# Optimization experiments

Hardware: AMD Instinct MI355X
Metric: run time of the kernel (lower is better)

The kernel has to match this reference:

```python
import jax, jax.numpy as jnp
import numpy as np


def _l2norm(t, eps=1e-12):
    # matches torch F.normalize(p=2, dim=-1): x / max(||x||_2, eps)
    n = jnp.sqrt(jnp.sum(t * t, axis=-1, keepdims=True))
    return t / jnp.maximum(n, eps)


def setup_inputs() -> dict:
    key = jax.random.key(0)
    ks = jax.random.split(key, 8)
    B, N, C, H, W = 16, 4, 256, 64, 64
    d = 64  # dim_head
    x = jax.random.normal(ks[0], (B, C, H, W), jnp.float32)
    fmaps = jax.random.normal(ks[1], (B, N, C, H, W), jnp.float32)
    Wq = jax.random.normal(ks[2], (N * d, C), jnp.float32) * 0.02   # Linear [out,in]
    Wk = jax.random.normal(ks[3], (N, d, C), jnp.float32) * 0.02    # grouped 1x1 conv, per-group [d,C]
    Wv = jax.random.normal(ks[4], (N, d, C), jnp.float32) * 0.02
    rescale = jnp.ones((N, 1, 1), jnp.float32)
    Wffn = jax.random.normal(ks[5], (C, N * d), jnp.float32) * 0.02
    bffn = jnp.zeros((C,), jnp.float32)
    return {"x": x, "fmaps": fmaps, "Wq": Wq, "Wk": Wk, "Wv": Wv,
            "rescale": rescale, "Wffn": Wffn, "bffn": bffn}


def reference(x, fmaps, Wq, Wk, Wv, rescale, Wffn, bffn):
    B, N, C, H, W = fmaps.shape
    d = Wk.shape[1]
    HW = H * W

    # x: [B,C,H,W] -> tokens [B,HW,C]
    x_in = jnp.transpose(x, (0, 2, 3, 1)).reshape(B, HW, C)
    q_in = jnp.einsum('bsc,oc->bso', x_in, Wq)            # [B,HW,N*d]

    # grouped 1x1 convs on fmaps (group = fmap index n)
    fm = fmaps.reshape(B, N, C, HW)                       # [B,N,C,HW]
    k = jnp.einsum('bncs,ndc->bnds', fm, Wk)              # [B,N,d,HW]
    v = jnp.einsum('bncs,ndc->bnds', fm, Wv)              # [B,N,d,HW]

    q = jnp.transpose(q_in.reshape(B, HW, N, d), (0, 2, 3, 1))  # [B,N,d,HW]

    qn = _l2norm(q)   # normalize over spatial (HW) axis
    kn = _l2norm(k)

    attn = jnp.einsum('bnds,bnes->bnde', kn, qn) * rescale      # [B,N,d,d]
    attn = jax.nn.softmax(attn, axis=-1)
    out = jnp.einsum('bnde,bnes->bnds', attn, v)                # [B,N,d,HW]

    out = jnp.transpose(out, (0, 3, 1, 2)).reshape(B, HW, N * d)  # [B,HW,N*d]
    out = out + q_in
    out = jnp.einsum('bsi,ci->bsc', out, Wffn) + bffn + q_in      # ffn + residual
    return jnp.transpose(out.reshape(B, H, W, C), (0, 3, 1, 2))   # [B,C,H,W]
```

## Files before the change

kernel.cpp:

```cpp
#include <hip/hip_runtime.h>
#include <hip/hip_bf16.h>
#include <cmath>

using bf16 = __hip_bfloat16;
typedef __attribute__((ext_vector_type(4))) float  f32x4;
typedef __attribute__((ext_vector_type(8))) short  bf16x8;
typedef unsigned int u32;
typedef unsigned short u16;

__device__ __forceinline__ void gl_lds16(const bf16* g, bf16* l) {
    __builtin_amdgcn_global_load_lds(
        (const __attribute__((address_space(1))) u32*)g,
        (__attribute__((address_space(3))) u32*)l, 16, 0, 0);
}

__device__ __forceinline__ u32 pk2(float a, float b) {
    bf16 ha = __float2bfloat16(a), hb = __float2bfloat16(b);
    return (u32)*(u16*)&ha | ((u32)*(u16*)&hb << 16);
}
__device__ __forceinline__ float b2f(u16 v) {
    return __uint_as_float((u32)v << 16);
}

__global__ __launch_bounds__(256) void qproj(
    const float* __restrict__ x,
    const bf16* __restrict__ Wq,
    bf16* __restrict__ qch)
{
    __shared__ bf16 sW[2][128 * 64];
    __shared__ bf16 sX[2][128 * 72];
    const int t = threadIdx.x;
    const int lane = t & 63, wid = t >> 6;
    const int wm = wid >> 1, wn = wid & 1;
    const int g = lane >> 4, lr = lane & 15;
    const int s0 = blockIdx.x * 128;
    const int o0 = blockIdx.y * 128;
    const float* xb = x + (long)blockIdx.z * 1048576;

    f32x4 acc[4][4];
#pragma unroll
    for (int i = 0; i < 4; ++i)
#pragma unroll
        for (int j = 0; j < 4; ++j) acc[i][j] = (f32x4){0.f, 0.f, 0.f, 0.f};

    const int p  = t & 31;
    const int sl = t >> 5;

    {
#pragma unroll
        for (int i = 0; i < 4; ++i) {
            int lin = i * 256 + t, r = lin >> 3, ch = lin & 7;
            gl_lds16(Wq + (long)(o0 + r) * 256 + ((ch ^ (r & 7)) << 3), &sW[0][lin * 8]);
        }
        float4 ra[4], rb[4];
#pragma unroll
        for (int j = 0; j < 4; ++j) {
            const float* src = xb + (long)(2 * p) * 4096 + s0 + (j * 8 + sl) * 4;
            ra[j] = *(const float4*)src;
            rb[j] = *(const float4*)(src + 4096);
        }
#pragma unroll
        for (int j = 0; j < 4; ++j) {
            char* base = (char*)&sX[0][0] + p * 4 + ((j * 8 + sl) * 4) * 144;
            *(u32*)(base +   0) = pk2(ra[j].x, rb[j].x);
            *(u32*)(base + 144) = pk2(ra[j].y, rb[j].y);
            *(u32*)(base + 288) = pk2(ra[j].z, rb[j].z);
            *(u32*)(base + 432) = pk2(ra[j].w, rb[j].w);
        }
        __syncthreads();
    }

    int cur = 0;
    for (int it = 0; it < 4; ++it) {
        const int c0n = (it + 1) * 64;
        float4 ra[4], rb[4];
        if (it < 3) {
#pragma unroll
            for (int i = 0; i < 4; ++i) {
                int lin = i * 256 + t, r = lin >> 3, ch = lin & 7;
                gl_lds16(Wq + (long)(o0 + r) * 256 + c0n + ((ch ^ (r & 7)) << 3),
                         &sW[cur ^ 1][lin * 8]);
            }
#pragma unroll
            for (int j = 0; j < 4; ++j) {
                const float* src = xb + (long)(c0n + 2 * p) * 4096 + s0 + (j * 8 + sl) * 4;
                ra[j] = *(const float4*)src;
                rb[j] = *(const float4*)(src + 4096);
            }
        }
        const char* wbase = (const char*)&sW[cur][0];
        const char* xbase = (const char*)&sX[cur][0];
#pragma unroll
        for (int kk = 0; kk < 2; ++kk) {
            bf16x8 aw[4], fx[4];
#pragma unroll
            for (int mf = 0; mf < 4; ++mf) {
                int r = wm * 64 + mf * 16 + lr;
                aw[mf] = *(const bf16x8*)(wbase + r * 128 + (((kk * 4 + g) ^ (r & 7)) << 4));
            }
#pragma unroll
            for (int nf = 0; nf < 4; ++nf) {
                int s = wn * 64 + nf * 16 + lr;
                fx[nf] = *(const bf16x8*)(xbase + s * 144 + (kk * 4 + g) * 16);
            }
#pragma unroll
            for (int mf = 0; mf < 4; ++mf)
#pragma unroll
                for (int nf = 0; nf < 4; ++nf)
                    acc[mf][nf] = __builtin_amdgcn_mfma_f32_16x16x32_bf16(
                        aw[mf], fx[nf], acc[mf][nf], 0, 0, 0);
        }
        if (it < 3) {
#pragma unroll
            for (int j = 0; j < 4; ++j) {
                char* base = (char*)&sX[cur ^ 1][0] + p * 4 + ((j * 8 + sl) * 4) * 144;
                *(u32*)(base +   0) = pk2(ra[j].x, rb[j].x);
                *(u32*)(base + 144) = pk2(ra[j].y, rb[j].y);
                *(u32*)(base + 288) = pk2(ra[j].z, rb[j].z);
                *(u32*)(base + 432) = pk2(ra[j].w, rb[j].w);
            }
            __syncthreads();
            cur ^= 1;
        }
    }

    bf16* qb = qch + (long)blockIdx.z * 1048576;
#pragma unroll
    for (int mf = 0; mf < 4; ++mf)
#pragma unroll
        for (int nf = 0; nf < 4; ++nf)
#pragma unroll
            for (int e = 0; e < 4; ++e) {
                int o = o0 + wm * 64 + mf * 16 + g * 4 + e;
                int s = s0 + wn * 64 + nf * 16 + lr;
                qb[(long)o * 4096 + s] = __float2bfloat16(acc[mf][nf][e]);
            }
}

__global__ __launch_bounds__(256) void kvproj(
    const float* __restrict__ fm,
    const bf16* __restrict__ Wk,
    const bf16* __restrict__ Wv,
    bf16* __restrict__ kb,
    bf16* __restrict__ vT)
{
    __shared__ bf16 sF[2][128 * 72];
    __shared__ bf16 sK[2][64 * 64];
    __shared__ bf16 sV[2][64 * 64];
    const int t = threadIdx.x;
    const int lane = t & 63, wid = t >> 6;
    const int g = lane >> 4, lr = lane & 15;
    const int s0 = blockIdx.x * 128;
    const int bn = blockIdx.y, n = bn & 3;
    const float* fb = fm + (long)bn * 1048576;
    const bf16* WkN = Wk + (long)n * 16384;
    const bf16* WvN = Wv + (long)n * 16384;

    f32x4 acc1[4][2];
    f32x4 acc2[2][4];
#pragma unroll
    for (int i = 0; i < 4; ++i)
#pragma unroll
        for (int j = 0; j < 2; ++j) {
            acc1[i][j] = (f32x4){0.f, 0.f, 0.f, 0.f};
            acc2[j][i] = (f32x4){0.f, 0.f, 0.f, 0.f};
        }

    const int p  = t & 31;
    const int sl = t >> 5;

    {
#pragma unroll
        for (int i = 0; i < 2; ++i) {
            int lin = i * 256 + t, r = lin >> 3, ch = lin & 7;
            int off = r * 256 + ((ch ^ (r & 7)) << 3);
            gl_lds16(WkN + off, &sK[0][lin * 8]);
            gl_lds16(WvN + off, &sV[0][lin * 8]);
        }
        float4 ra[4], rb[4];
#pragma unroll
        for (int j = 0; j < 4; ++j) {
            const float* src = fb + (long)(2 * p) * 4096 + s0 + (j * 8 + sl) * 4;
            ra[j] = *(const float4*)src;
            rb[j] = *(const float4*)(src + 4096);
        }
#pragma unroll
        for (int j = 0; j < 4; ++j) {
            char* base = (char*)&sF[0][0] + p * 4 + ((j * 8 + sl) * 4) * 144;
            *(u32*)(base +   0) = pk2(ra[j].x, rb[j].x);
            *(u32*)(base + 144) = pk2(ra[j].y, rb[j].y);
            *(u32*)(base + 288) = pk2(ra[j].z, rb[j].z);
            *(u32*)(base + 432) = pk2(ra[j].w, rb[j].w);
        }
        __syncthreads();
    }

    int cur = 0;
    for (int it = 0; it < 4; ++it) {
        const int c0n = (it + 1) * 64;
        float4 ra[4], rb[4];
        if (it < 3) {
#pragma unroll
            for (int i = 0; i < 2; ++i) {
                int lin = i * 256 + t, r = lin >> 3, ch = lin & 7;
                int off = r * 256 + c0n + ((ch ^ (r & 7)) << 3);
                gl_lds16(WkN + off, &sK[cur ^ 1][lin * 8]);
                gl_lds16(WvN + off, &sV[cur ^ 1][lin * 8]);
            }
#pragma unroll
            for (int j = 0; j < 4; ++j) {
                const float* src = fb + (long)(c0n + 2 * p) * 4096 + s0 + (j * 8 + sl) * 4;
                ra[j] = *(const float4*)src;
                rb[j] = *(const float4*)(src + 4096);
            }
        }
        const char* fbase = (const char*)&sF[cur][0];
        const char* kbase = (const char*)&sK[cur][0];
        const char* vbase = (const char*)&sV[cur][0];
#pragma unroll
        for (int kk = 0; kk < 2; ++kk) {
            bf16x8 ak[4], ff[2], bv[4];
#pragma unroll
            for (int mf = 0; mf < 4; ++mf) {
                int r = mf * 16 + lr;
                ak[mf] = *(const bf16x8*)(kbase + r * 128 + (((kk * 4 + g) ^ (r & 7)) << 4));
            }
#pragma unroll
            for (int i = 0; i < 2; ++i) {
                int s = wid * 32 + i * 16 + lr;
                ff[i] = *(const bf16x8*)(fbase + s * 144 + (kk * 4 + g) * 16);
            }
#pragma unroll
            for (int nf = 0; nf < 4; ++nf) {
                int r = nf * 16 + lr;
                bv[nf] = *(const bf16x8*)(vbase + r * 128 + (((kk * 4 + g) ^ (r & 7)) << 4));
            }
#pragma unroll
            for (int mf = 0; mf < 4; ++mf)
#pragma unroll
                for (int i = 0; i < 2; ++i)
                    acc1[mf][i] = __builtin_amdgcn_mfma_f32_16x16x32_bf16(
                        ak[mf], ff[i], acc1[mf][i], 0, 0, 0);
#pragma unroll
            for (int i = 0; i < 2; ++i)
#pragma unroll
                for (int nf = 0; nf < 4; ++nf)
                    acc2[i][nf] = __builtin_amdgcn_mfma_f32_16x16x32_bf16(
                        ff[i], bv[nf], acc2[i][nf], 0, 0, 0);
        }
        if (it < 3) {
#pragma unroll
            for (int j = 0; j < 4; ++j) {
                char* base = (char*)&sF[cur ^ 1][0] + p * 4 + ((j * 8 + sl) * 4) * 144;
                *(u32*)(base +   0) = pk2(ra[j].x, rb[j].x);
                *(u32*)(base + 144) = pk2(ra[j].y, rb[j].y);
                *(u32*)(base + 288) = pk2(ra[j].z, rb[j].z);
                *(u32*)(base + 432) = pk2(ra[j].w, rb[j].w);
            }
            __syncthreads();
            cur ^= 1;
        }
    }

    bf16* kbb = kb + (long)bn * 262144;
#pragma unroll
    for (int mf = 0; mf < 4; ++mf)
#pragma unroll
        for (int i = 0; i < 2; ++i)
#pragma unroll
            for (int e = 0; e < 4; ++e) {
                int dd = mf * 16 + g * 4 + e;
                int s  = s0 + wid * 32 + i * 16 + lr;
                kbb[(long)dd * 4096 + s] = __float2bfloat16(acc1[mf][i][e]);
            }
    bf16* vtb = vT + (long)bn * 262144;
#pragma unroll
    for (int i = 0; i < 2; ++i)
#pragma unroll
        for (int nf = 0; nf < 4; ++nf)
#pragma unroll
            for (int e = 0; e < 4; ++e) {
                int s = s0 + wid * 32 + i * 16 + g * 4 + e;
                int ec = nf * 16 + lr;
                vtb[(long)s * 64 + ec] = __float2bfloat16(acc2[i][nf][e]);
            }
}

__global__ __launch_bounds__(256) void qk_sum(
    const bf16* __restrict__ kb,
    const bf16* __restrict__ qch,
    float* __restrict__ part,
    float* __restrict__ sumq, float* __restrict__ sumk)
{
    __shared__ bf16 sA[2][64 * 64];
    __shared__ bf16 sB[2][64 * 64];
    const int t = threadIdx.x;
    const int lane = t & 63, wid = t >> 6;
    const int wm = wid >> 1, wn = wid & 1;
    const int g = lane >> 4, lr = lane & 15;
    const int ch_ = blockIdx.x;
    const int bn = blockIdx.y;
    const bf16* kbase = kb + (long)bn * 262144;
    const bf16* qbase = qch + (long)bn * 262144;

    const int srow = t >> 1;
    const int shalf = t & 1;

    f32x4 acc[2][2];
#pragma unroll
    for (int i = 0; i < 2; ++i)
#pragma unroll
        for (int j = 0; j < 2; ++j) acc[i][j] = (f32x4){0.f, 0.f, 0.f, 0.f};
    float ss = 0.f;

    {
        int k0 = ch_ * 512;
#pragma unroll
        for (int i = 0; i < 2; ++i) {
            int lin = i * 256 + t, r = lin >> 3, c = lin & 7;
            gl_lds16(kbase + (long)r * 4096 + k0 + ((c ^ (r & 7)) << 3), &sA[0][lin * 8]);
            gl_lds16(qbase + (long)r * 4096 + k0 + ((c ^ (r & 7)) << 3), &sB[0][lin * 8]);
        }
        __syncthreads();
    }

    int cur = 0;
    for (int it = 0; it < 8; ++it) {
        if (it < 7) {
            int k0 = ch_ * 512 + (it + 1) * 64;
#pragma unroll
            for (int i = 0; i < 2; ++i) {
                int lin = i * 256 + t, r = lin >> 3, c = lin & 7;
                gl_lds16(kbase + (long)r * 4096 + k0 + ((c ^ (r & 7)) << 3), &sA[cur ^ 1][lin * 8]);
                gl_lds16(qbase + (long)r * 4096 + k0 + ((c ^ (r & 7)) << 3), &sB[cur ^ 1][lin * 8]);
            }
        }
        const char* abase = (const char*)&sA[cur][0];
        const char* bbase = (const char*)&sB[cur][0];
#pragma unroll
        for (int kk = 0; kk < 2; ++kk) {
            bf16x8 af[2], bf[2];
#pragma unroll
            for (int mf = 0; mf < 2; ++mf) {
                int r = wm * 32 + mf * 16 + lr;
                af[mf] = *(const bf16x8*)(abase + r * 128 + (((kk * 4 + g) ^ (r & 7)) << 4));
            }
#pragma unroll
            for (int nf = 0; nf < 2; ++nf) {
                int r = wn * 32 + nf * 16 + lr;
                bf[nf] = *(const bf16x8*)(bbase + r * 128 + (((kk * 4 + g) ^ (r & 7)) << 4));
            }
#pragma unroll
            for (int mf = 0; mf < 2; ++mf)
#pragma unroll
                for (int nf = 0; nf < 2; ++nf)
                    acc[mf][nf] = __builtin_amdgcn_mfma_f32_16x16x32_bf16(
                        af[mf], bf[nf], acc[mf][nf], 0, 0, 0);
        }
        {
            const char* base = (srow < 64) ? abase + srow * 128
                                           : bbase + (srow - 64) * 128;
            int r7 = srow & 7;
#pragma unroll
            for (int j = 0; j < 4; ++j) {
                bf16x8 v = *(const bf16x8*)(base + (((shalf * 4 + j) ^ r7) << 4));
#pragma unroll
                for (int e = 0; e < 8; ++e) {
                    float f = b2f((u16)v[e]);
                    ss += f * f;
                }
            }
        }
        __syncthreads();
        cur ^= 1;
    }

    ss += __shfl_xor(ss, 1);
    if (shalf == 0) {
        if (srow < 64) sumk[ch_ * 4096 + bn * 64 + srow] = ss;
        else           sumq[ch_ * 4096 + bn * 64 + srow - 64] = ss;
    }
    float* pp = part + ((long)bn * 8 + ch_) * 4096;
#pragma unroll
    for (int mf = 0; mf < 2; ++mf)
#pragma unroll
        for (int nf = 0; nf < 2; ++nf)
#pragma unroll
            for (int e = 0; e < 4; ++e) {
                int m = wm * 32 + mf * 16 + g * 4 + e;
                int nn = wn * 32 + nf * 16 + lr;
                pp[m * 64 + nn] = acc[mf][nf][e];
            }
}

__global__ __launch_bounds__(256) void attn_finalize_kernel(
    const float* __restrict__ part,
    const float* __restrict__ sumq, const float* __restrict__ sumk,
    const float* __restrict__ rescale,
    bf16* __restrict__ attn_out)
{
    const int bn = blockIdx.x;
    const int n = bn & 3;
    const int t = threadIdx.x;
    const float rs = rescale[n];

    __shared__ float att[64][65];
    __shared__ float rmax[64], rsum[64];
    __shared__ float iq[64], ik[64];

    if (t < 64) {
        float s = 0.f;
#pragma unroll
        for (int c = 0; c < 8; ++c) s += sumk[c * 4096 + bn * 64 + t];
        ik[t] = 1.f / fmaxf(sqrtf(s), 1e-12f);
    } else if (t < 128) {
        float s = 0.f;
#pragma unroll
        for (int c = 0; c < 8; ++c) s += sumq[c * 4096 + bn * 64 + t - 64];
        iq[t - 64] = 1.f / fmaxf(sqrtf(s), 1e-12f);
    }
    __syncthreads();

    const float* pb = part + (size_t)bn * 8 * 4096;
#pragma unroll
    for (int p = 0; p < 16; ++p) {
        int lin = p * 256 + t;
        int dd = lin >> 6, e = lin & 63;
        float v = 0.f;
#pragma unroll
        for (int c = 0; c < 8; ++c) v += pb[c * 4096 + lin];
        v *= ik[dd] * iq[e] * rs;
        att[dd][e] = v;
    }
    __syncthreads();
    if (t < 64) {
        float m = -1e30f;
        for (int e = 0; e < 64; ++e) m = fmaxf(m, att[t][e]);
        float sm = 0.f;
        for (int e = 0; e < 64; ++e) sm += expf(att[t][e] - m);
        rmax[t] = m;
        rsum[t] = 1.0f / sm;
    }
    __syncthreads();
    bf16* ob = attn_out + (size_t)bn * 4096;
#pragma unroll
    for (int p = 0; p < 16; ++p) {
        int lin = p * 256 + t;
        int dd = lin >> 6, e = lin & 63;
        ob[lin] = __float2bfloat16(expf(att[dd][e] - rmax[dd]) * rsum[dd]);
    }
}

__global__ __launch_bounds__(256) void pvffn(
    const bf16* __restrict__ vT,
    const bf16* __restrict__ attnb,
    const bf16* __restrict__ qch,
    const bf16* __restrict__ Wf,
    const float* __restrict__ bffn,
    float* __restrict__ out)
{
    __shared__ bf16 bufA[2][12288];
    __shared__ bf16 Zs[128 * 64];
    const int t = threadIdx.x;
    const int lane = t & 63, wid = t >> 6;
    const int g = lane >> 4, lr = lane & 15;
    const int s0 = blockIdx.x * 128;
    const int b = blockIdx.y;

    f32x4 accF[4][8];
#pragma unroll
    for (int i = 0; i < 4; ++i)
#pragma unroll
        for (int j = 0; j < 8; ++j) accF[i][j] = (f32x4){0.f, 0.f, 0.f, 0.f};

    {
        const int bn = b * 4;
#pragma unroll
        for (int i = 0; i < 4; ++i) {
            int lin = i * 256 + t, r = lin >> 3, c = lin & 7;
            gl_lds16(vT + (long)bn * 262144 + (long)(s0 + r) * 64 + ((c ^ (r & 7)) << 3),
                     &bufA[0][lin * 8]);
        }
#pragma unroll
        for (int i = 0; i < 2; ++i) {
            int lin = i * 256 + t, r = lin >> 3, c = lin & 7;
            gl_lds16(attnb + (long)bn * 4096 + r * 64 + ((c ^ (r & 7)) << 3),
                     &bufA[0][8192 + lin * 8]);
        }
        __syncthreads();
    }

    for (int n = 0; n < 4; ++n) {
        const int bn = b * 4 + n;
        const int cur = n & 1;
        if (n < 3) {
            const int bnn = bn + 1;
#pragma unroll
            for (int i = 0; i < 4; ++i) {
                int lin = i * 256 + t, r = lin >> 3, c = lin & 7;
                gl_lds16(vT + (long)bnn * 262144 + (long)(s0 + r) * 64 + ((c ^ (r & 7)) << 3),
                         &bufA[cur ^ 1][lin * 8]);
            }
#pragma unroll
            for (int i = 0; i < 2; ++i) {
                int lin = i * 256 + t, r = lin >> 3, c = lin & 7;
                gl_lds16(attnb + (long)bnn * 4096 + r * 64 + ((c ^ (r & 7)) << 3),
                         &bufA[cur ^ 1][8192 + lin * 8]);
            }
        }
        bf16x8 wf[2][4];
#pragma unroll
        for (int kk = 0; kk < 2; ++kk)
#pragma unroll
            for (int mf = 0; mf < 4; ++mf)
                wf[kk][mf] = *(const bf16x8*)(
                    Wf + (long)(wid * 64 + mf * 16 + lr) * 256 + n * 64 + (kk * 4 + g) * 8);

        const char* vb = (const char*)&bufA[cur][0];
        const char* ab = vb + 16384;
        f32x4 accP[2][4];
#pragma unroll
        for (int i = 0; i < 2; ++i)
#pragma unroll
            for (int j = 0; j < 4; ++j) accP[i][j] = (f32x4){0.f, 0.f, 0.f, 0.f};
#pragma unroll
        for (int kk = 0; kk < 2; ++kk) {
            bf16x8 av[2], at[4];
#pragma unroll
            for (int mf = 0; mf < 2; ++mf) {
                int r = wid * 32 + mf * 16 + lr;
                av[mf] = *(const bf16x8*)(vb + r * 128 + (((kk * 4 + g) ^ (r & 7)) << 4));
            }
#pragma unroll
            for (int nf = 0; nf < 4; ++nf) {
                int r = nf * 16 + lr;
                at[nf] = *(const bf16x8*)(ab + r * 128 + (((kk * 4 + g) ^ (r & 7)) << 4));
            }
#pragma unroll
            for (int mf = 0; mf < 2; ++mf)
#pragma unroll
                for (int nf = 0; nf < 4; ++nf)
                    accP[mf][nf] = __builtin_amdgcn_mfma_f32_16x16x32_bf16(
                        av[mf], at[nf], accP[mf][nf], 0, 0, 0);
        }
#pragma unroll
        for (int mf = 0; mf < 2; ++mf)
#pragma unroll
            for (int nf = 0; nf < 4; ++nf) {
                int slb = wid * 32 + mf * 16 + g * 4;
                int il = nf * 16 + lr;
                ushort4 qv = *(const ushort4*)(qch + ((long)b * 256 + n * 64 + il) * 4096 + s0 + slb);
                u16 qa[4] = {qv.x, qv.y, qv.z, qv.w};
#pragma unroll
                for (int e = 0; e < 4; ++e) {
                    int sl = slb + e;
                    float v = accP[mf][nf][e] + b2f(qa[e]);
                    bf16 hv = __float2bfloat16(v);
                    int byte = sl * 128 + ((((il >> 3) ^ (sl & 7))) << 4) + (il & 7) * 2;
                    *(u16*)((char*)Zs + byte) = *(u16*)&hv;
                }
            }
        __syncthreads();
#pragma unroll
        for (int kk = 0; kk < 2; ++kk) {
            bf16x8 bz[8];
#pragma unroll
            for (int nf = 0; nf < 8; ++nf) {
                int sl = nf * 16 + lr;
                bz[nf] = *(const bf16x8*)((const char*)Zs + sl * 128 + (((kk * 4 + g) ^ (sl & 7)) << 4));
            }
#pragma unroll
            for (int mf = 0; mf < 4; ++mf)
#pragma unroll
                for (int nf = 0; nf < 8; ++nf)
                    accF[mf][nf] = __builtin_amdgcn_mfma_f32_16x16x32_bf16(
                        wf[kk][mf], bz[nf], accF[mf][nf], 0, 0, 0);
        }
        __syncthreads();
    }

    float* ob = out + (long)b * 1048576;
    const bf16* qb = qch + (long)b * 1048576;
#pragma unroll
    for (int mf = 0; mf < 4; ++mf)
#pragma unroll
        for (int e = 0; e < 4; ++e) {
            int c = wid * 64 + mf * 16 + g * 4 + e;
            float bv = bffn[c];
#pragma unroll
            for (int nf = 0; nf < 8; ++nf) {
                int s = s0 + nf * 16 + lr;
                long idx = (long)c * 4096 + s;
                ob[idx] = accF[mf][nf][e] + bv + b2f(*(const u16*)(qb + idx));
            }
        }
}

__global__ __launch_bounds__(256) void wconv(
    const float* __restrict__ a, const float* __restrict__ b,
    const float* __restrict__ c, const float* __restrict__ d,
    bf16* __restrict__ o)
{
    int i = blockIdx.x * 256 + threadIdx.x;
    int which = i >> 16, off = i & 65535;
    const float* s = (which == 0) ? a : (which == 1) ? b : (which == 2) ? c : d;
    o[i] = __float2bfloat16(s[off]);
}

extern "C" void kernel_launch(void* const* d_in, const int* in_sizes, int n_in,
                              void* d_out, int out_size, void* d_ws, size_t ws_size,
                              hipStream_t stream) {
    const float* x       = (const float*)d_in[0];
    const float* fmaps   = (const float*)d_in[1];
    const float* Wq      = (const float*)d_in[2];
    const float* Wk      = (const float*)d_in[3];
    const float* Wv      = (const float*)d_in[4];
    const float* rescale = (const float*)d_in[5];
    const float* Wffn    = (const float*)d_in[6];
    const float* bffn    = (const float*)d_in[7];
    float* out = (float*)d_out;

    char* w = (char*)d_ws;
    bf16* kbuf  = (bf16*)(w + 0);
    bf16* vT    = (bf16*)(w + 33554432L);
    bf16* qch   = (bf16*)(w + 67108864L);
    float* part = (float*)(w + 100663296L);
    bf16* attnb = (bf16*)(w + 109051904L);
    float* sumq = (float*)(w + 109576192L);
    float* sumk = (float*)(w + 109707264L);
    bf16* Wq_b  = (bf16*)(w + 109838336L);
    bf16* Wk_b  = Wq_b + 65536;
    bf16* Wv_b  = Wq_b + 131072;
    bf16* Wf_b  = Wq_b + 196608;

    dim3 blk(256);

    wconv<<<dim3(1024), blk, 0, stream>>>(Wq, Wk, Wv, Wffn, Wq_b);
    kvproj<<<dim3(32, 64), blk, 0, stream>>>(fmaps, Wk_b, Wv_b, kbuf, vT);
    qproj<<<dim3(32, 2, 16), blk, 0, stream>>>(x, Wq_b, qch);
    qk_sum<<<dim3(8, 64), blk, 0, stream>>>(kbuf, qch, part, sumq, sumk);
    attn_finalize_kernel<<<dim3(64), blk, 0, stream>>>(part, sumq, sumk, rescale, attnb);
    pvffn<<<dim3(32, 16), blk, 0, stream>>>(vT, attnb, qch, Wf_b, bffn, out);
}
```

Measured before the change: 194.2 us.

## Widen qproj to 512 threads covering all output channels per block

The Q projection now uses 512-thread blocks, each covering all 256 output channels for a 128-token tile, so the fp32 x tile is loaded and converted to bf16 once instead of once per output half. The double-buffered prefetch pipeline is replaced by a single-buffered load-sync-compute loop. This halves redundant reads of x, but drops the overlap of global loads with MFMA work and adds a barrier per K step.

```diff
diff --git a/kernel.cpp b/kernel.cpp
--- a/kernel.cpp
+++ b/kernel.cpp
@@ -22,20 +22,20 @@
     return __uint_as_float((u32)v << 16);
 }
 
-__global__ __launch_bounds__(256) void qproj(
+__global__ __launch_bounds__(512) void qproj8(
     const float* __restrict__ x,
     const bf16* __restrict__ Wq,
     bf16* __restrict__ qch)
 {
-    __shared__ bf16 sW[2][128 * 64];
-    __shared__ bf16 sX[2][128 * 72];
+    __shared__ __align__(16) bf16 sW[256 * 64];
+    __shared__ __align__(16) bf16 sX[128 * 72];
     const int t = threadIdx.x;
     const int lane = t & 63, wid = t >> 6;
     const int wm = wid >> 1, wn = wid & 1;
     const int g = lane >> 4, lr = lane & 15;
     const int s0 = blockIdx.x * 128;
-    const int o0 = blockIdx.y * 128;
-    const float* xb = x + (long)blockIdx.z * 1048576;
+    const int b = blockIdx.y;
+    const float* xb = x + (long)b * 1048576;
 
     f32x4 acc[4][4];
 #pragma unroll
@@ -46,62 +46,38 @@
     const int p  = t & 31;
     const int sl = t >> 5;
 
-    {
+    for (int c0 = 0; c0 < 256; c0 += 64) {
+        __syncthreads();
 #pragma unroll
         for (int i = 0; i < 4; ++i) {
-            int lin = i * 256 + t, r = lin >> 3, ch = lin & 7;
-            gl_lds16(Wq + (long)(o0 + r) * 256 + ((ch ^ (r & 7)) << 3), &sW[0][lin * 8]);
-        }
-        float4 ra[4], rb[4];
-#pragma unroll
-        for (int j = 0; j < 4; ++j) {
-            const float* src = xb + (long)(2 * p) * 4096 + s0 + (j * 8 + sl) * 4;
-            ra[j] = *(const float4*)src;
-            rb[j] = *(const float4*)(src + 4096);
-        }
-#pragma unroll
-        for (int j = 0; j < 4; ++j) {
-            char* base = (char*)&sX[0][0] + p * 4 + ((j * 8 + sl) * 4) * 144;
-            *(u32*)(base +   0) = pk2(ra[j].x, rb[j].x);
-            *(u32*)(base + 144) = pk2(ra[j].y, rb[j].y);
-            *(u32*)(base + 288) = pk2(ra[j].z, rb[j].z);
-            *(u32*)(base + 432) = pk2(ra[j].w, rb[j].w);
-        }
-        __syncthreads();
-    }
-
-    int cur = 0;
-    for (int it = 0; it < 4; ++it) {
-        const int c0n = (it + 1) * 64;
-        float4 ra[4], rb[4];
-        if (it < 3) {
-#pragma unroll
-            for (int i = 0; i < 4; ++i) {
-                int lin = i * 256 + t, r = lin >> 3, ch = lin & 7;
-                gl_lds16(Wq + (long)(o0 + r) * 256 + c0n + ((ch ^ (r & 7)) << 3),
-                         &sW[cur ^ 1][lin * 8]);
-            }
-#pragma unroll
-            for (int j = 0; j < 4; ++j) {
-                const float* src = xb + (long)(c0n + 2 * p) * 4096 + s0 + (j * 8 + sl) * 4;
-                ra[j] = *(const float4*)src;
-                rb[j] = *(const float4*)(src + 4096);
-            }
-        }
-        const char* wbase = (const char*)&sW[cur][0];
-        const char* xbase = (const char*)&sX[cur][0];
+            int lin = i * 512 + t, r = lin >> 3, ch = lin & 7;
+            gl_lds16(Wq + (long)r * 256 + c0 + ((ch ^ (r & 7)) << 3), &sW[lin * 8]);
+        }
+#pragma unroll
+        for (int j = 0; j < 2; ++j) {
+            int s4 = j * 16 + sl;
+            const float* src = xb + (long)(c0 + 2 * p) * 4096 + s0 + s4 * 4;
+            float4 a = *(const float4*)src;
+            float4 bq = *(const float4*)(src + 4096);
+            char* base = (char*)sX + p * 4 + (s4 * 4) * 144;
+            *(u32*)(base +   0) = pk2(a.x, bq.x);
+            *(u32*)(base + 144) = pk2(a.y, bq.y);
+            *(u32*)(base + 288) = pk2(a.z, bq.z);
+            *(u32*)(base + 432) = pk2(a.w, bq.w);
+        }
+        __syncthreads();
 #pragma unroll
         for (int kk = 0; kk < 2; ++kk) {
             bf16x8 aw[4], fx[4];
 #pragma unroll
             for (int mf = 0; mf < 4; ++mf) {
                 int r = wm * 64 + mf * 16 + lr;
-                aw[mf] = *(const bf16x8*)(wbase + r * 128 + (((kk * 4 + g) ^ (r & 7)) << 4));
+                aw[mf] = *(const bf16x8*)((const char*)sW + r * 128 + (((kk * 4 + g) ^ (r & 7)) << 4));
             }
 #pragma unroll
             for (int nf = 0; nf < 4; ++nf) {
                 int s = wn * 64 + nf * 16 + lr;
-                fx[nf] = *(const bf16x8*)(xbase + s * 144 + (kk * 4 + g) * 16);
+                fx[nf] = *(const bf16x8*)((const char*)sX + s * 144 + (kk * 4 + g) * 16);
             }
 #pragma unroll
             for (int mf = 0; mf < 4; ++mf)
@@ -110,28 +86,15 @@
                     acc[mf][nf] = __builtin_amdgcn_mfma_f32_16x16x32_bf16(
                         aw[mf], fx[nf], acc[mf][nf], 0, 0, 0);
         }
-        if (it < 3) {
-#pragma unroll
-            for (int j = 0; j < 4; ++j) {
-                char* base = (char*)&sX[cur ^ 1][0] + p * 4 + ((j * 8 + sl) * 4) * 144;
-                *(u32*)(base +   0) = pk2(ra[j].x, rb[j].x);
-                *(u32*)(base + 144) = pk2(ra[j].y, rb[j].y);
-                *(u32*)(base + 288) = pk2(ra[j].z, rb[j].z);
-                *(u32*)(base + 432) = pk2(ra[j].w, rb[j].w);
-            }
-            __syncthreads();
-            cur ^= 1;
-        }
-    }
-
-    bf16* qb = qch + (long)blockIdx.z * 1048576;
+    }
+    bf16* qb = qch + (long)b * 1048576;
 #pragma unroll
     for (int mf = 0; mf < 4; ++mf)
 #pragma unroll
         for (int nf = 0; nf < 4; ++nf)
 #pragma unroll
             for (int e = 0; e < 4; ++e) {
-                int o = o0 + wm * 64 + mf * 16 + g * 4 + e;
+                int o = wm * 64 + mf * 16 + g * 4 + e;
                 int s = s0 + wn * 64 + nf * 16 + lr;
                 qb[(long)o * 4096 + s] = __float2bfloat16(acc[mf][nf][e]);
             }
@@ -637,7 +600,7 @@
 
     wconv<<<dim3(1024), blk, 0, stream>>>(Wq, Wk, Wv, Wffn, Wq_b);
     kvproj<<<dim3(32, 64), blk, 0, stream>>>(fmaps, Wk_b, Wv_b, kbuf, vT);
-    qproj<<<dim3(32, 2, 16), blk, 0, stream>>>(x, Wq_b, qch);
+    qproj8<<<dim3(32, 16), dim3(512), 0, stream>>>(x, Wq_b, qch);
     qk_sum<<<dim3(8, 64), blk, 0, stream>>>(kbuf, qch, part, sumq, sumk);
     attn_finalize_kernel<<<dim3(64), blk, 0, stream>>>(part, sumq, sumk, rescale, attnb);
     pvffn<<<dim3(32, 16), blk, 0, stream>>>(vT, attnb, qch, Wf_b, bffn, out);
```

After: 184.0 us. -5.2%, faster.
